# Optimization experiments

Hardware: AMD Instinct MI355X
Metric: run time of the kernel (lower is better)

The kernel has to match this reference:

```python
import jax, jax.numpy as jnp
import numpy as np

B, S, C, H, RANK = 8, 1024, 1280, 8, 4
MERGE_SCALE = 1.0   # self.scale
LORA_SCALE = 1.0    # scale arg passed to __call__ (defaults 1.0)


def setup_inputs() -> dict:
    key = jax.random.key(0)
    ks = jax.random.split(key, 20)
    std = 1.0 / np.sqrt(C)
    rstd = 1.0 / np.sqrt(RANK)
    d = {
        "hidden_states": jax.random.normal(ks[0], (B, S, C), jnp.float32),
        "pose_feature": jax.random.normal(ks[1], (B, S, C), jnp.float32),
        # qkv_merge Linear (init to zeros in the module; use small random to exercise the path)
        "qkv_merge_w": jax.random.normal(ks[2], (C, C), jnp.float32) * (0.02 * std),
        "qkv_merge_b": jax.random.normal(ks[3], (C,), jnp.float32) * 0.01,
        # attn.to_q/k/v (bias-free, diffusers default) and to_out[0] (with bias). Stored [in, out].
        "wq": jax.random.normal(ks[4], (C, C), jnp.float32) * std,
        "wk": jax.random.normal(ks[5], (C, C), jnp.float32) * std,
        "wv": jax.random.normal(ks[6], (C, C), jnp.float32) * std,
        "wo": jax.random.normal(ks[7], (C, C), jnp.float32) * std,
        "bo": jax.random.normal(ks[8], (C,), jnp.float32) * 0.01,
        # LoRA layers: down [in, rank], up [rank, out] (up is zeros at init; random here)
        "q_lora_down": jax.random.normal(ks[9], (C, RANK), jnp.float32) * std,
        "q_lora_up": jax.random.normal(ks[10], (RANK, C), jnp.float32) * rstd,
        "k_lora_down": jax.random.normal(ks[11], (C, RANK), jnp.float32) * std,
        "k_lora_up": jax.random.normal(ks[12], (RANK, C), jnp.float32) * rstd,
        "v_lora_down": jax.random.normal(ks[13], (C, RANK), jnp.float32) * std,
        "v_lora_up": jax.random.normal(ks[14], (RANK, C), jnp.float32) * rstd,
        "out_lora_down": jax.random.normal(ks[15], (C, RANK), jnp.float32) * std,
        "out_lora_up": jax.random.normal(ks[16], (RANK, C), jnp.float32) * rstd,
        "num_heads": H,
    }
    return d


def _lora(x, down, up):
    # LoRALinearLayer with network_alpha=None -> scale factor 1
    return (x @ down) @ up


def reference(hidden_states, pose_feature, qkv_merge_w, qkv_merge_b,
              wq, wk, wv, wo, bo,
              q_lora_down, q_lora_up, k_lora_down, k_lora_up,
              v_lora_down, v_lora_up, out_lora_down, out_lora_up,
              num_heads):
    b, s, c = hidden_states.shape
    dh = c // num_heads
    # gated pose-merge (query_condition and key_value_condition -> shared qkv source)
    merged = (hidden_states + pose_feature) @ qkv_merge_w + qkv_merge_b
    x = merged * MERGE_SCALE + hidden_states  # [b, s, c]
    # LoRA-augmented projections
    q = x @ wq + LORA_SCALE * _lora(x, q_lora_down, q_lora_up)
    k = x @ wk + LORA_SCALE * _lora(x, k_lora_down, k_lora_up)
    v = x @ wv + LORA_SCALE * _lora(x, v_lora_down, v_lora_up)
    # head_to_batch_dim -> [b, h, s, dh]
    q = q.reshape(b, s, num_heads, dh).transpose(0, 2, 1, 3)
    k = k.reshape(b, s, num_heads, dh).transpose(0, 2, 1, 3)
    v = v.reshape(b, s, num_heads, dh).transpose(0, 2, 1, 3)
    # attn.get_attention_scores: baddbmm scaled by head_dim**-0.5, then softmax
    scores = jnp.einsum('bhqd,bhkd->bhqk', q, k) * (dh ** -0.5)
    probs = jax.nn.softmax(scores, axis=-1)
    out = jnp.einsum('bhqk,bhkd->bhqd', probs, v)
    # batch_to_head_dim -> [b, s, c]
    out = out.transpose(0, 2, 1, 3).reshape(b, s, c)
    # output projection + LoRA; to_out[1] is dropout (identity at eval)
    out = out @ wo + bo + LORA_SCALE * _lora(out, out_lora_down, out_lora_up)
    # residual_connection=False, rescale_output_factor=1.0
    return out
```

## Files before the change

### kernel.cpp

```cpp
#include <hip/hip_runtime.h>
#include <stdint.h>

typedef unsigned short u16;
typedef __attribute__((ext_vector_type(8))) short short8;
typedef __attribute__((ext_vector_type(4))) float f32x4;

__device__ __forceinline__ float b2f(u16 x){
  union { unsigned u; float f; } v; v.u = ((unsigned)x) << 16; return v.f;
}
__device__ __forceinline__ float b2fs(short x){ return b2f((u16)x); }
__device__ __forceinline__ u16 f2b(float f){
  union { float f; unsigned u; } v; v.f = f;
  unsigned u = v.u;
  u += 0x7FFFu + ((u >> 16) & 1u);
  return (u16)(u >> 16);
}
__device__ __forceinline__ float ldg_f(const void* p, int i, int f32){
  return f32 ? ((const float*)p)[i] : b2f(((const u16*)p)[i]);
}
__device__ __forceinline__ void gld16(const void* g, void* l){
  __builtin_amdgcn_global_load_lds(
      (__attribute__((address_space(1))) void*)(g),
      (__attribute__((address_space(3))) void*)(l), 16, 0, 0);
}

__global__ void detect_dtype(const u16* __restrict__ hid, int* __restrict__ flag){
  if (blockIdx.x == 0){
    int lane = threadIdx.x & 63;
    int plaus = 0;
    for (int i = lane; i < 512; i += 64){
      u16 v = hid[2 * i];
      int e = (v >> 7) & 0xFF;
      if ((e >= 100 && e <= 140) || (v & 0x7FFF) == 0) plaus++;
    }
    #pragma unroll
    for (int xm = 1; xm < 64; xm <<= 1) plaus += __shfl_xor(plaus, xm, 64);
    if (threadIdx.x == 0) *flag = (plaus < 400) ? 1 : 0;
  }
}

__global__ void make_t(const void* __restrict__ hid, const void* __restrict__ pose,
                       u16* __restrict__ t, const int* __restrict__ flag){
  int base = (blockIdx.x * 256 + threadIdx.x) * 8;
  short8 o;
  if (*flag){
    #pragma unroll
    for (int j = 0; j < 2; j++){
      float4 a = *(const float4*)((const float*)hid  + base + j * 4);
      float4 b = *(const float4*)((const float*)pose + base + j * 4);
      o[j * 4 + 0] = (short)f2b(a.x + b.x);
      o[j * 4 + 1] = (short)f2b(a.y + b.y);
      o[j * 4 + 2] = (short)f2b(a.z + b.z);
      o[j * 4 + 3] = (short)f2b(a.w + b.w);
    }
  } else {
    short8 a = *(const short8*)((const u16*)hid  + base);
    short8 b = *(const short8*)((const u16*)pose + base);
    #pragma unroll
    for (int j = 0; j < 8; j++) o[j] = (short)f2b(b2fs(a[j]) + b2fs(b[j]));
  }
  *(short8*)(t + base) = o;
}

__global__ void prep_w(const void* __restrict__ w, const void* __restrict__ dn,
                       const void* __restrict__ up, u16* __restrict__ WT,
                       int rowOff, float sc, const int* __restrict__ flag)
{
  __shared__ float tile[64][65];
  const int f = *flag;
  const int k0 = blockIdx.x * 64, n0 = blockIdx.y * 64;
  const int tr  = threadIdx.x >> 2;
  const int tc0 = (threadIdx.x & 3) * 16;
  #pragma unroll
  for (int i = 0; i < 16; i++)
    tile[tr][tc0 + i] = ldg_f(w, (k0 + tr) * 1280 + n0 + tc0 + i, f);
  __syncthreads();
  const int n = n0 + tr;
  float upv[4];
  if (dn){
    #pragma unroll
    for (int r = 0; r < 4; r++) upv[r] = ldg_f(up, r * 1280 + n, f);
  }
  u16 tmp[16];
  #pragma unroll
  for (int i = 0; i < 16; i++){
    int k = k0 + tc0 + i;
    float val = tile[tc0 + i][tr];
    if (dn){
      #pragma unroll
      for (int r = 0; r < 4; r++)
        val += ldg_f(dn, k * 4 + r, f) * upv[r];
    }
    tmp[i] = f2b(val * sc);
  }
  u16* dst = &WT[(rowOff + n) * 1280 + k0 + tc0];
  #pragma unroll
  for (int i = 0; i < 4; i++)
    *(ushort4*)(dst + i * 4) = *(ushort4*)(tmp + i * 4);
}

#define GPHASE(KK, MH)                                                         \
  {                                                                            \
    if ((MH) == 0){                                                            \
      _Pragma("unroll")                                                        \
      for (int n = 0; n < 4; n++){                                             \
        int R = wn * 64 + n * 16 + l15;                                        \
        int c = (KK) * 32 + quad * 8;                                          \
        bfr[n] = *(const short8*)&Bsm[b][R * 64 + (c ^ (((R >> 2) & 1) << 4))];\
      }                                                                        \
    }                                                                          \
    short8 af[4];                                                              \
    _Pragma("unroll")                                                          \
    for (int j = 0; j < 4; j++){                                               \
      int R = wm * 128 + ((MH) * 4 + j) * 16 + l15;                            \
      int c = (KK) * 32 + quad * 8;                                            \
      af[j] = *(const short8*)&Asm[b][R * 64 + (c ^ (((R >> 2) & 1) << 4))];   \
    }                                                                          \
    __builtin_amdgcn_s_barrier();                                              \
    asm volatile("s_waitcnt lgkmcnt(0)" ::: "memory");                         \
    __builtin_amdgcn_s_setprio(1);                                             \
    _Pragma("unroll")                                                          \
    for (int j = 0; j < 4; j++)                                                \
      _Pragma("unroll")                                                        \
      for (int n = 0; n < 4; n++)                                              \
        acc[(MH) * 4 + j][n] = __builtin_amdgcn_mfma_f32_16x16x32_bf16(        \
            af[j], bfr[n], acc[(MH) * 4 + j][n], 0, 0, 0);                     \
    __builtin_amdgcn_s_setprio(0);                                             \
    __builtin_amdgcn_s_barrier();                                              \
  }

template<bool BIAS, bool RESID, bool RAWOUT, bool VSPLIT>
__global__ __launch_bounds__(512, 2) void gemm256(
    const u16* __restrict__ A, const u16* __restrict__ BT,
    const void* __restrict__ bias, const void* __restrict__ resid,
    void* __restrict__ Cout, u16* __restrict__ vtg,
    int gridX, int NOUT, int Kdim, const int* __restrict__ flag)
{
  __shared__ alignas(16) u16 Asm[2][256 * 64];
  __shared__ alignas(16) u16 Bsm[2][256 * 64];
  const int tid  = threadIdx.x;
  const int lane = tid & 63;
  const int w    = tid >> 6;
  const int wm   = w >> 2, wn = w & 3;
  const int quad = lane >> 4, l15 = lane & 15;

  const int nwg = gridDim.x;
  const int id  = blockIdx.x;
  const int swz = (id & 7) * (nwg >> 3) + (id >> 3);
  const int bx  = swz % gridX;
  const int by  = swz / gridX;
  const int tileM = by << 8;
  const int tileN = bx << 8;
  const int f32 = (BIAS || RESID || RAWOUT) ? *flag : 0;

  auto stageHalf = [&](int bufi, int half, int kt){
    const int k0 = kt << 6;
    #pragma unroll
    for (int s = 0; s < 2; s++){
      int cl  = s * 512 + tid;
      int p   = ((half & 1) << 10) + cl;
      int lc  = p ^ (((p >> 5) & 1) << 1);
      int row = lc >> 3, slot = lc & 7;
      if (half < 2)
        gld16(&A [(tileM + row) * Kdim + k0 + slot * 8], (char*)Asm[bufi] + p * 16);
      else
        gld16(&BT[(tileN + row) * Kdim + k0 + slot * 8], (char*)Bsm[bufi] + p * 16);
    }
  };

  f32x4 acc[8][4];
  #pragma unroll
  for (int mi = 0; mi < 8; mi++)
    #pragma unroll
    for (int ni = 0; ni < 4; ni++)
      acc[mi][ni] = (f32x4){0.f, 0.f, 0.f, 0.f};

  const int NT = Kdim >> 6;
  stageHalf(0, 0, 0); stageHalf(0, 1, 0); stageHalf(0, 2, 0); stageHalf(0, 3, 0);
  stageHalf(1, 0, 1); stageHalf(1, 1, 1);
  asm volatile("s_waitcnt vmcnt(4)" ::: "memory");
  __builtin_amdgcn_s_barrier();

  for (int kt = 0; kt < NT; kt++){
    const int b = kt & 1;
    short8 bfr[4];
    if (kt + 1 < NT) stageHalf(b ^ 1, 2, kt + 1);
    GPHASE(0, 0)
    if (kt + 1 < NT) stageHalf(b ^ 1, 3, kt + 1);
    GPHASE(0, 1)
    GPHASE(1, 0)
    GPHASE(1, 1)
    if (kt + 2 < NT){ stageHalf(b, 0, kt + 2); stageHalf(b, 1, kt + 2); }
    if (kt + 1 < NT){
      if (kt + 2 < NT) asm volatile("s_waitcnt vmcnt(4)" ::: "memory");
      else             asm volatile("s_waitcnt vmcnt(0)" ::: "memory");
      __builtin_amdgcn_s_barrier();
    }
  }

  if (VSPLIT && tileN >= 2560){
    #pragma unroll
    for (int mi = 0; mi < 8; mi++){
      #pragma unroll
      for (int ni = 0; ni < 4; ni++){
        int col = tileN + wn * 64 + ni * 16 + l15;
        int hd = col - 2560;
        int hh = hd / 160;
        int dd = hd - hh * 160;
        int row0 = tileM + wm * 128 + mi * 16 + quad * 4;
        int bb = row0 >> 10;
        long addr = ((long)((bb * 8 + hh) * 160 + dd) << 10) | (long)(row0 & 1023);
        ushort4 pk;
        pk.x = f2b(acc[mi][ni][0]); pk.y = f2b(acc[mi][ni][1]);
        pk.z = f2b(acc[mi][ni][2]); pk.w = f2b(acc[mi][ni][3]);
        *(ushort4*)&vtg[addr] = pk;
      }
    }
  } else {
    #pragma unroll
    for (int mi = 0; mi < 8; mi++){
      #pragma unroll
      for (int ni = 0; ni < 4; ni++){
        int col = tileN + wn * 64 + ni * 16 + l15;
        float bv = 0.f;
        if (BIAS) bv = ldg_f(bias, col, f32);
        #pragma unroll
        for (int r = 0; r < 4; r++){
          int row = tileM + wm * 128 + mi * 16 + quad * 4 + r;
          float v = acc[mi][ni][r] + bv;
          if (RESID) v += ldg_f(resid, row * NOUT + col, f32);
          if (RAWOUT && f32) ((float*)Cout)[row * NOUT + col] = v;
          else               ((u16*)Cout)[row * NOUT + col]   = f2b(v);
        }
      }
    }
  }
}

__global__ __launch_bounds__(256, 2) void attn_mfma(
    const u16* __restrict__ qk, const u16* __restrict__ vtg,
    u16* __restrict__ out)
{
  __shared__ alignas(16) u16 Ks[2 * 64 * 160];
  __shared__ alignas(16) u16 Vt[160 * 64];
  __shared__ alignas(16) u16 Ps[4 * 32 * 72];

  const int tid  = threadIdx.x, lane = tid & 63, wv = tid >> 6;
  const int quad = lane >> 4,   l15  = lane & 15;
  const int bh = ((blockIdx.y >> 3) << 3) | blockIdx.x;
  const int qt = blockIdx.y & 7;
  const int b  = bh >> 3, h = bh & 7;
  const int rowBase = (b << 10) + (qt << 7);
  const int kBase   = b << 10;

  short8 qa[2][5];
  #pragma unroll
  for (int mi = 0; mi < 2; mi++)
    #pragma unroll
    for (int kk = 0; kk < 5; kk++)
      qa[mi][kk] = *(const short8*)&qk[
          (rowBase + wv * 32 + mi * 16 + l15) * 2560 + h * 160 + kk * 32 + quad * 8];

  f32x4 o[2][10];
  #pragma unroll
  for (int mi = 0; mi < 2; mi++)
    #pragma unroll
    for (int ni = 0; ni < 10; ni++)
      o[mi][ni] = (f32x4){0.f, 0.f, 0.f, 0.f};
  float mr[2][4], lr[2][4];
  #pragma unroll
  for (int mi = 0; mi < 2; mi++)
    #pragma unroll
    for (int r = 0; r < 4; r++){ mr[mi][r] = -1e30f; lr[mi][r] = 0.f; }

  #pragma unroll
  for (int i = 0; i < 5; i++){
    int c = tid + (i << 8);
    int kr = c / 20, kc = c % 20;
    gld16(&qk[(kBase + kr) * 2560 + 1280 + h * 160 + (kc << 3)],
          (char*)Ks + c * 16);
  }
  __syncthreads();

  int buf = 0;
  for (int kt = 0; kt < 16; kt++){
    #pragma unroll
    for (int i = 0; i < 5; i++){
      int c = tid + (i << 8);
      int d = c >> 3;
      int l = (c & 7) ^ (d & 7);
      gld16(&vtg[((bh * 160 + d) << 10) + (kt << 6) + (l << 3)],
            (char*)Vt + c * 16);
    }
    if (kt < 15){
      #pragma unroll
      for (int i = 0; i < 5; i++){
        int c = tid + (i << 8);
        int kr = c / 20, kc = c % 20;
        gld16(&qk[(kBase + ((kt + 1) << 6) + kr) * 2560 + 1280 + h * 160 + (kc << 3)],
              (char*)Ks + (buf ^ 1) * 20480 + c * 16);
      }
    }
    const u16* KsR = Ks + buf * 10240;

    f32x4 s[2][4];
    #pragma unroll
    for (int mi = 0; mi < 2; mi++)
      #pragma unroll
      for (int ni = 0; ni < 4; ni++)
        s[mi][ni] = (f32x4){0.f, 0.f, 0.f, 0.f};
    __builtin_amdgcn_s_setprio(1);
    #pragma unroll
    for (int kk = 0; kk < 5; kk++){
      #pragma unroll
      for (int ni = 0; ni < 4; ni++){
        short8 bf = *(const short8*)&KsR[(ni * 16 + l15) * 160 + kk * 32 + quad * 8];
        s[0][ni] = __builtin_amdgcn_mfma_f32_16x16x32_bf16(qa[0][kk], bf, s[0][ni], 0, 0, 0);
        s[1][ni] = __builtin_amdgcn_mfma_f32_16x16x32_bf16(qa[1][kk], bf, s[1][ni], 0, 0, 0);
      }
    }
    __builtin_amdgcn_s_setprio(0);

    float al[2][4];
    #pragma unroll
    for (int mi = 0; mi < 2; mi++){
      #pragma unroll
      for (int r = 0; r < 4; r++){
        float mx = fmaxf(fmaxf(s[mi][0][r], s[mi][1][r]),
                         fmaxf(s[mi][2][r], s[mi][3][r]));
        #pragma unroll
        for (int xm = 1; xm < 16; xm <<= 1) mx = fmaxf(mx, __shfl_xor(mx, xm, 64));
        float mn = fmaxf(mr[mi][r], mx);
        float a  = __expf(mr[mi][r] - mn);
        mr[mi][r] = mn; al[mi][r] = a;
        float sum = 0.f;
        #pragma unroll
        for (int ni = 0; ni < 4; ni++){
          float p = __expf(s[mi][ni][r] - mn);
          s[mi][ni][r] = p; sum += p;
        }
        #pragma unroll
        for (int xm = 1; xm < 16; xm <<= 1) sum += __shfl_xor(sum, xm, 64);
        lr[mi][r] = lr[mi][r] * a + sum;
      }
    }
    #pragma unroll
    for (int mi = 0; mi < 2; mi++)
      #pragma unroll
      for (int ni = 0; ni < 4; ni++)
        #pragma unroll
        for (int r = 0; r < 4; r++)
          Ps[wv * 2304 + (mi * 16 + quad * 4 + r) * 72 + ni * 16 + l15] =
              f2b(s[mi][ni][r]);
    #pragma unroll
    for (int mi = 0; mi < 2; mi++)
      #pragma unroll
      for (int ni = 0; ni < 10; ni++)
        #pragma unroll
        for (int r = 0; r < 4; r++)
          o[mi][ni][r] *= al[mi][r];

    if (kt < 15) asm volatile("s_waitcnt vmcnt(5)" ::: "memory");
    else         asm volatile("s_waitcnt vmcnt(0)" ::: "memory");
    __builtin_amdgcn_s_barrier();

    __builtin_amdgcn_s_setprio(1);
    #pragma unroll
    for (int kk2 = 0; kk2 < 2; kk2++){
      short8 pa0 = *(const short8*)&Ps[wv * 2304 + l15 * 72        + kk2 * 32 + quad * 8];
      short8 pa1 = *(const short8*)&Ps[wv * 2304 + (16 + l15) * 72 + kk2 * 32 + quad * 8];
      #pragma unroll
      for (int ni = 0; ni < 10; ni++){
        short8 vf = *(const short8*)&Vt[((ni * 16 + l15) << 6) +
                                        (((((kk2 << 2) | quad)) ^ (l15 & 7)) << 3)];
        o[0][ni] = __builtin_amdgcn_mfma_f32_16x16x32_bf16(pa0, vf, o[0][ni], 0, 0, 0);
        o[1][ni] = __builtin_amdgcn_mfma_f32_16x16x32_bf16(pa1, vf, o[1][ni], 0, 0, 0);
      }
    }
    __builtin_amdgcn_s_setprio(0);

    asm volatile("s_waitcnt vmcnt(0)" ::: "memory");
    __builtin_amdgcn_s_barrier();
    buf ^= 1;
  }

  #pragma unroll
  for (int mi = 0; mi < 2; mi++){
    #pragma unroll
    for (int r = 0; r < 4; r++){
      float inv = 1.0f / lr[mi][r];
      int row = rowBase + wv * 32 + mi * 16 + quad * 4 + r;
      #pragma unroll
      for (int ni = 0; ni < 10; ni++)
        out[row * 1280 + h * 160 + ni * 16 + l15] = f2b(o[mi][ni][r] * inv);
    }
  }
}

extern "C" void kernel_launch(void* const* d_in, const int* in_sizes, int n_in,
                              void* d_out, int out_size, void* d_ws, size_t ws_size,
                              hipStream_t stream)
{
  const void* hid  = d_in[0];
  const void* pose = d_in[1];
  const void* wm   = d_in[2];
  const void* mb   = d_in[3];
  const void* wq   = d_in[4];
  const void* wk   = d_in[5];
  const void* wv   = d_in[6];
  const void* wo   = d_in[7];
  const void* bo   = d_in[8];
  const void* qd   = d_in[9];
  const void* qu   = d_in[10];
  const void* kd   = d_in[11];
  const void* ku   = d_in[12];
  const void* vd   = d_in[13];
  const void* vu   = d_in[14];
  const void* od   = d_in[15];
  const void* ou   = d_in[16];
  (void)in_sizes; (void)n_in; (void)out_size; (void)ws_size;

  u16* ws   = (u16*)d_ws;
  u16* qk   = ws;
  u16* t    = qk;
  u16* x    = qk + 20971520;
  u16* vtg  = x + 10485760;
  u16* Wbuf = vtg + 10485760;
  u16* attnout = x;
  int* flag = (int*)(Wbuf + 4915200);

  const float qscale = 0.07905694150420949f;

  detect_dtype<<<1, 64, 0, stream>>>((const u16*)hid, flag);
  make_t<<<5120, 256, 0, stream>>>(hid, pose, t, flag);
  prep_w<<<dim3(20, 20), 256, 0, stream>>>(wm, nullptr, nullptr, Wbuf, 0, 1.0f, flag);
  gemm256<true, true, false, false><<<160, 512, 0, stream>>>(
      t, Wbuf, mb, hid, x, nullptr, 5, 1280, 1280, flag);
  prep_w<<<dim3(20, 20), 256, 0, stream>>>(wq, qd, qu, Wbuf, 0, qscale, flag);
  prep_w<<<dim3(20, 20), 256, 0, stream>>>(wk, kd, ku, Wbuf, 1280, 1.0f, flag);
  prep_w<<<dim3(20, 20), 256, 0, stream>>>(wv, vd, vu, Wbuf, 2560, 1.0f, flag);
  gemm256<false, false, false, true><<<480, 512, 0, stream>>>(
      x, Wbuf, nullptr, nullptr, qk, vtg, 15, 2560, 1280, flag);
  attn_mfma<<<dim3(8, 64), 256, 0, stream>>>(qk, vtg, attnout);
  prep_w<<<dim3(20, 20), 256, 0, stream>>>(wo, od, ou, Wbuf, 0, 1.0f, flag);
  gemm256<true, false, true, false><<<160, 512, 0, stream>>>(
      attnout, Wbuf, bo, nullptr, d_out, nullptr, 5, 1280, 1280, flag);
}
```

Before: 577.0 us.

## Use 128x128 GEMM for square projections and stronger LDS swizzle in QKV GEMM

The merge and output projections (N=1280) move from the 256x256 pipelined kernel, which launched only 160 blocks, to a simpler 128x128-tile kernel with 640 blocks. The aim is to fill the GPU's compute units better. The large QKV GEMM keeps the 256-tile kernel, specialised to drop its unused epilogue branches, and switches to a full XOR-by-row swizzle of the LDS slot index to cut bank conflicts. The new small kernel has no double buffering and syncs twice per 32-wide k-step, so its per-block efficiency is lower.

```diff
diff --git a/kernel.cpp b/kernel.cpp
--- a/kernel.cpp
+++ b/kernel.cpp
@@ -99,22 +99,92 @@
     *(ushort4*)(dst + i * 4) = *(ushort4*)(tmp + i * 4);
 }
 
+template<bool BIAS, bool RESID, bool RAWOUT>
+__global__ __launch_bounds__(256) void gemm_bt(
+    const u16* __restrict__ A, const u16* __restrict__ BT,
+    const void* __restrict__ bias, const void* __restrict__ resid,
+    void* __restrict__ Cout, int NOUT, int Kdim, const int* __restrict__ flag)
+{
+  __shared__ alignas(16) u16 As[128 * 32];
+  __shared__ alignas(16) u16 Bs[128 * 32];
+  const int tid  = threadIdx.x;
+  const int lane = tid & 63;
+  const int w    = tid >> 6;
+  const int wm   = w >> 1, wn = w & 1;
+  const int quad = lane >> 4, l15 = lane & 15;
+  const int tileM = blockIdx.y << 7;
+  const int tileN = blockIdx.x << 7;
+  const int f32 = (BIAS || RESID || RAWOUT) ? *flag : 0;
+
+  f32x4 acc[4][4];
+  #pragma unroll
+  for (int mi = 0; mi < 4; mi++)
+    #pragma unroll
+    for (int ni = 0; ni < 4; ni++)
+      acc[mi][ni] = (f32x4){0.f, 0.f, 0.f, 0.f};
+
+  for (int k0 = 0; k0 < Kdim; k0 += 32){
+    {
+      int c = tid;
+      gld16(&A [(tileM + (c >> 2)) * Kdim + k0 + ((c & 3) << 3)], (char*)As + c * 16);
+      gld16(&BT[(tileN + (c >> 2)) * Kdim + k0 + ((c & 3) << 3)], (char*)Bs + c * 16);
+      c = tid + 256;
+      gld16(&A [(tileM + (c >> 2)) * Kdim + k0 + ((c & 3) << 3)], (char*)As + c * 16);
+      gld16(&BT[(tileN + (c >> 2)) * Kdim + k0 + ((c & 3) << 3)], (char*)Bs + c * 16);
+    }
+    __syncthreads();
+
+    short8 af[4], bfr[4];
+    #pragma unroll
+    for (int mi = 0; mi < 4; mi++)
+      af[mi] = *(const short8*)(As + (wm * 64 + mi * 16 + l15) * 32 + quad * 8);
+    #pragma unroll
+    for (int ni = 0; ni < 4; ni++)
+      bfr[ni] = *(const short8*)(Bs + (wn * 64 + ni * 16 + l15) * 32 + quad * 8);
+    #pragma unroll
+    for (int mi = 0; mi < 4; mi++)
+      #pragma unroll
+      for (int ni = 0; ni < 4; ni++)
+        acc[mi][ni] = __builtin_amdgcn_mfma_f32_16x16x32_bf16(
+            af[mi], bfr[ni], acc[mi][ni], 0, 0, 0);
+    __syncthreads();
+  }
+
+  #pragma unroll
+  for (int mi = 0; mi < 4; mi++){
+    #pragma unroll
+    for (int ni = 0; ni < 4; ni++){
+      int col = tileN + wn * 64 + ni * 16 + l15;
+      float bv = 0.f;
+      if (BIAS) bv = ldg_f(bias, col, f32);
+      #pragma unroll
+      for (int r = 0; r < 4; r++){
+        int row = tileM + wm * 64 + mi * 16 + quad * 4 + r;
+        float v = acc[mi][ni][r] + bv;
+        if (RESID) v += ldg_f(resid, row * NOUT + col, f32);
+        if (RAWOUT && f32) ((float*)Cout)[row * NOUT + col] = v;
+        else               ((u16*)Cout)[row * NOUT + col]   = f2b(v);
+      }
+    }
+  }
+}
+
 #define GPHASE(KK, MH)                                                         \
   {                                                                            \
     if ((MH) == 0){                                                            \
       _Pragma("unroll")                                                        \
       for (int n = 0; n < 4; n++){                                             \
         int R = wn * 64 + n * 16 + l15;                                        \
-        int c = (KK) * 32 + quad * 8;                                          \
-        bfr[n] = *(const short8*)&Bsm[b][R * 64 + (c ^ (((R >> 2) & 1) << 4))];\
+        int sl = (KK) * 4 + quad;                                              \
+        bfr[n] = *(const short8*)&Bsm[b][R * 64 + ((sl ^ (R & 7)) << 3)];      \
       }                                                                        \
     }                                                                          \
     short8 af[4];                                                              \
     _Pragma("unroll")                                                          \
     for (int j = 0; j < 4; j++){                                               \
       int R = wm * 128 + ((MH) * 4 + j) * 16 + l15;                            \
-      int c = (KK) * 32 + quad * 8;                                            \
-      af[j] = *(const short8*)&Asm[b][R * 64 + (c ^ (((R >> 2) & 1) << 4))];   \
+      int sl = (KK) * 4 + quad;                                                \
+      af[j] = *(const short8*)&Asm[b][R * 64 + ((sl ^ (R & 7)) << 3)];         \
     }                                                                          \
     __builtin_amdgcn_s_barrier();                                              \
     asm volatile("s_waitcnt lgkmcnt(0)" ::: "memory");                         \
@@ -129,12 +199,10 @@
     __builtin_amdgcn_s_barrier();                                              \
   }
 
-template<bool BIAS, bool RESID, bool RAWOUT, bool VSPLIT>
-__global__ __launch_bounds__(512, 2) void gemm256(
+__global__ __launch_bounds__(512, 2) void gemm256_qkv(
     const u16* __restrict__ A, const u16* __restrict__ BT,
-    const void* __restrict__ bias, const void* __restrict__ resid,
-    void* __restrict__ Cout, u16* __restrict__ vtg,
-    int gridX, int NOUT, int Kdim, const int* __restrict__ flag)
+    u16* __restrict__ Cout, u16* __restrict__ vtg,
+    int gridX, int Kdim)
 {
   __shared__ alignas(16) u16 Asm[2][256 * 64];
   __shared__ alignas(16) u16 Bsm[2][256 * 64];
@@ -151,20 +219,19 @@
   const int by  = swz / gridX;
   const int tileM = by << 8;
   const int tileN = bx << 8;
-  const int f32 = (BIAS || RESID || RAWOUT) ? *flag : 0;
 
   auto stageHalf = [&](int bufi, int half, int kt){
     const int k0 = kt << 6;
     #pragma unroll
     for (int s = 0; s < 2; s++){
-      int cl  = s * 512 + tid;
-      int p   = ((half & 1) << 10) + cl;
-      int lc  = p ^ (((p >> 5) & 1) << 1);
-      int row = lc >> 3, slot = lc & 7;
+      int cl   = s * 512 + tid;
+      int p    = ((half & 1) << 10) + cl;
+      int row  = p >> 3;
+      int lslt = (p & 7) ^ (row & 7);
       if (half < 2)
-        gld16(&A [(tileM + row) * Kdim + k0 + slot * 8], (char*)Asm[bufi] + p * 16);
+        gld16(&A [(tileM + row) * Kdim + k0 + lslt * 8], (char*)Asm[bufi] + p * 16);
       else
-        gld16(&BT[(tileN + row) * Kdim + k0 + slot * 8], (char*)Bsm[bufi] + p * 16);
+        gld16(&BT[(tileN + row) * Kdim + k0 + lslt * 8], (char*)Bsm[bufi] + p * 16);
     }
   };
 
@@ -198,7 +265,7 @@
     }
   }
 
-  if (VSPLIT && tileN >= 2560){
+  if (tileN >= 2560){
     #pragma unroll
     for (int mi = 0; mi < 8; mi++){
       #pragma unroll
@@ -222,15 +289,10 @@
       #pragma unroll
       for (int ni = 0; ni < 4; ni++){
         int col = tileN + wn * 64 + ni * 16 + l15;
-        float bv = 0.f;
-        if (BIAS) bv = ldg_f(bias, col, f32);
         #pragma unroll
         for (int r = 0; r < 4; r++){
           int row = tileM + wm * 128 + mi * 16 + quad * 4 + r;
-          float v = acc[mi][ni][r] + bv;
-          if (RESID) v += ldg_f(resid, row * NOUT + col, f32);
-          if (RAWOUT && f32) ((float*)Cout)[row * NOUT + col] = v;
-          else               ((u16*)Cout)[row * NOUT + col]   = f2b(v);
+          Cout[row * 2560 + col] = f2b(acc[mi][ni][r]);
         }
       }
     }
@@ -434,15 +496,14 @@
   detect_dtype<<<1, 64, 0, stream>>>((const u16*)hid, flag);
   make_t<<<5120, 256, 0, stream>>>(hid, pose, t, flag);
   prep_w<<<dim3(20, 20), 256, 0, stream>>>(wm, nullptr, nullptr, Wbuf, 0, 1.0f, flag);
-  gemm256<true, true, false, false><<<160, 512, 0, stream>>>(
-      t, Wbuf, mb, hid, x, nullptr, 5, 1280, 1280, flag);
+  gemm_bt<true, true, false><<<dim3(10, 64), 256, 0, stream>>>(
+      t, Wbuf, mb, hid, x, 1280, 1280, flag);
   prep_w<<<dim3(20, 20), 256, 0, stream>>>(wq, qd, qu, Wbuf, 0, qscale, flag);
   prep_w<<<dim3(20, 20), 256, 0, stream>>>(wk, kd, ku, Wbuf, 1280, 1.0f, flag);
   prep_w<<<dim3(20, 20), 256, 0, stream>>>(wv, vd, vu, Wbuf, 2560, 1.0f, flag);
-  gemm256<false, false, false, true><<<480, 512, 0, stream>>>(
-      x, Wbuf, nullptr, nullptr, qk, vtg, 15, 2560, 1280, flag);
+  gemm256_qkv<<<480, 512, 0, stream>>>(x, Wbuf, qk, vtg, 15, 1280);
   attn_mfma<<<dim3(8, 64), 256, 0, stream>>>(qk, vtg, attnout);
   prep_w<<<dim3(20, 20), 256, 0, stream>>>(wo, od, ou, Wbuf, 0, 1.0f, flag);
-  gemm256<true, false, true, false><<<160, 512, 0, stream>>>(
-      attnout, Wbuf, bo, nullptr, d_out, nullptr, 5, 1280, 1280, flag);
-}
+  gemm_bt<true, false, true><<<dim3(10, 64), 256, 0, stream>>>(
+      attnout, Wbuf, bo, nullptr, d_out, 1280, 1280, flag);
+}
```

Result: faster. 536.0 us (-7.1%).
